# Optimization experiments

Hardware: AMD Instinct MI355X
Metric: run time of the kernel (lower is better)

Reference implementation:

```python
import jax, jax.numpy as jnp
import numpy as np

# Fixed generation configuration (original samples num_nodes per graph from
# dataset stats; here batched with fixed node count so shapes are static).
B, N = 64, 384                 # num_graphs, nodes per graph
NOISE, CED, HID, FEAT, NCLS = 128, 64, 512, 256, 10
DENSITY = 0.05                 # fallback density used by the original code
TEMP = 1.0                     # temperature
IU, JU = np.triu_indices(N, k=1)   # all i<j pairs, matches nested loop order
P = IU.shape[0]                # pairs per graph = N*(N-1)/2
K = int(round(DENSITY * P))    # topk edges per graph


def setup_inputs() -> dict:
    key = jax.random.key(0)
    ks = jax.random.split(key, 8)
    f32 = jnp.float32
    return {
        "z": jax.random.normal(ks[0], (B, N, NOISE), f32),
        "class_labels": jax.random.randint(ks[1], (B,), 0, NCLS),
        "embed_table": jax.random.normal(ks[2], (NCLS, CED), f32),
        "W1": jax.random.normal(ks[3], (NOISE + CED, HID), f32) / np.float32(np.sqrt(NOISE + CED)),
        "b1": jnp.zeros((HID,), f32),
        "W2": jax.random.normal(ks[4], (HID, FEAT), f32) / np.float32(np.sqrt(HID)),
        "b2": jnp.zeros((FEAT,), f32),
        "We": jax.random.normal(ks[5], (FEAT, HID), f32) / np.float32(np.sqrt(FEAT)),
        "be": jnp.zeros((HID,), f32),
        "threshold": jnp.float32(1.0),
    }


def reference(z, class_labels, embed_table, W1, b1, W2, b2, We, be, threshold):
    # class embedding, broadcast to every node of the graph
    ce = embed_table[class_labels]                               # [B, CED]
    ce = jnp.broadcast_to(ce[:, None, :], (B, N, CED))
    inp = jnp.concatenate([z, ce], axis=-1)                      # [B, N, NOISE+CED]
    # node generator: Linear -> ReLU -> Linear
    x = jax.nn.relu(inp @ W1 + b1) @ W2 + b2                     # [B, N, FEAT]
    # edge predictor encoder: Linear -> ReLU
    h = jax.nn.relu(x @ We + be)                                 # [B, N, HID]
    # pairwise L2 distances via gram trick (replaces O(n^2) torch.norm loop)
    sq = jnp.sum(h * h, axis=-1)                                 # [B, N]
    gram = jnp.einsum('bnd,bmd->bnm', h, h)                      # [B, N, N]
    d2 = jnp.maximum(sq[:, :, None] + sq[:, None, :] - 2.0 * gram, 0.0)
    dist = jnp.sqrt(jnp.maximum(d2[:, IU, JU], 1e-12))           # [B, P] upper-tri pairs
    probs = jax.nn.sigmoid((threshold - dist) / max(TEMP, 1e-6)) # [B, P]
    # per-graph top-k edge selection
    top_probs, top_idx = jax.lax.top_k(probs, K)                 # [B, K]
    iu = jnp.asarray(IU, jnp.int32)
    ju = jnp.asarray(JU, jnp.int32)
    offs = (jnp.arange(B, dtype=jnp.int32) * N)[:, None]         # node offset per graph
    u = iu[top_idx] + offs                                       # [B, K]
    v = ju[top_idx] + offs
    # per graph: [[u, v], [v, u]] (symmetrized), graphs concatenated
    row0 = jnp.concatenate([u, v], axis=1).reshape(-1)           # [B*2K]
    row1 = jnp.concatenate([v, u], axis=1).reshape(-1)
    edge_index = jnp.stack([row0, row1], axis=0)                 # [2, B*2K]
    batch = jnp.repeat(jnp.arange(B, dtype=jnp.int32), N)        # [B*N]
    return x.reshape(B * N, FEAT), edge_index, batch, top_probs
```

## Files before the change

kernel.cpp:

```cpp
#include <hip/hip_runtime.h>
#include <hip/hip_bf16.h>

#define NB    64
#define NN    384
#define PPAIR 73536
#define PRECT 147456
#define KSEL  3677
#define NSLICE 8
#define SLICEK (PRECT / NSLICE)

#define OFF_X 0
#define OFF_E 6291456
#define B2K   470656
#define OFF_B 7232768
#define OFF_P 7257344
#define TOT   7492672

#define WS_H8    0ull
#define WS_GH    0ull
#define WS_SB    4194304ull
#define WS_SQ    12582912ull
#define WS_W1P   12681216ull
#define WS_W2P   12877824ull
#define WS_WEP   13139968ull
#define WS_KEY   13402112ull
#define WS_SEL   38567936ull
#define WS_TB    39509248ull

typedef __attribute__((ext_vector_type(8))) short bf16x8;
typedef __attribute__((ext_vector_type(4))) float f32x4;

__device__ __forceinline__ short f2bf(float f) {
    __hip_bfloat16 h = __float2bfloat16(f);
    return *reinterpret_cast<short*>(&h);
}
__device__ __forceinline__ unsigned enc8(float h) {
    if (!(h > 0.0078125f)) return 0u;
    unsigned u = __float_as_uint(h) + 0x00080000u;
    int E = (int)(u >> 23) - 127;
    if (E > 8)  return 0x7Eu;
    if (E < -6) return 0u;
    return (unsigned)(((E + 7) << 3) | ((u >> 20) & 7u));
}
__device__ __forceinline__ float dec8(unsigned b) {
    if (b == 0u) return 0.f;
    return __uint_as_float((((b >> 3) + 120u) << 23) | ((b & 7u) << 20));
}

__device__ __forceinline__ void bar_lds() {
    asm volatile("s_waitcnt lgkmcnt(0)\n\ts_barrier" ::: "memory");
}

__device__ __forceinline__ int4 pack8bf(const float4& A, const float4& B) {
    int4 v;
    v.x = (unsigned short)f2bf(A.x) | ((unsigned)(unsigned short)f2bf(A.y) << 16);
    v.y = (unsigned short)f2bf(A.z) | ((unsigned)(unsigned short)f2bf(A.w) << 16);
    v.z = (unsigned short)f2bf(B.x) | ((unsigned)(unsigned short)f2bf(B.y) << 16);
    v.w = (unsigned short)f2bf(B.z) | ((unsigned)(unsigned short)f2bf(B.w) << 16);
    return v;
}

__device__ __forceinline__ void packOne(
    const float* __restrict__ W, int K, int N, short* __restrict__ dst, int idx)
{
    if (idx >= K * N) return;
    int j = idx & 7;
    int l = (idx >> 3) & 63;
    int rest = idx >> 9;
    int Kt = K >> 5;
    int kt = rest % Kt, mt = rest / Kt;
    int k = kt * 32 + (l >> 4) * 8 + j;
    int n = mt * 16 + (l & 15);
    dst[idx] = f2bf(W[(size_t)k * N + n]);
}

__global__ __launch_bounds__(256) void pack_all_kernel(
    const float* __restrict__ W1, const float* __restrict__ W2,
    const float* __restrict__ We, short* __restrict__ W1p,
    short* __restrict__ W2p, short* __restrict__ Wep, float* __restrict__ sqW)
{
    int blk = blockIdx.x, tid = threadIdx.x;
    if (blk < 384)        packOne(W1, 192, 512, W1p, blk * 256 + tid);
    else if (blk < 896)   packOne(W2, 512, 256, W2p, (blk - 384) * 256 + tid);
    else if (blk < 1408)  packOne(We, 256, 512, Wep, (blk - 896) * 256 + tid);
    else {
        int i = (blk - 1408) * 256 + tid;
        if (i < NB * NN) sqW[i] = 0.f;
    }
}

__global__ __launch_bounds__(256, 3) void fused_mlp_kernel(
    const float* __restrict__ z, const int* __restrict__ cls,
    const float* __restrict__ et,
    const short* __restrict__ W1p, const float* __restrict__ b1,
    const short* __restrict__ W2p, const float* __restrict__ b2,
    const short* __restrict__ Wep, const float* __restrict__ be,
    float* __restrict__ xOut, unsigned char* __restrict__ h8Out,
    float* __restrict__ sqOut)
{
    extern __shared__ short lds[];
    short* A_lds  = lds;
    short* t1_lds = lds + 6400;
    short* x_lds  = lds;

    const int tid = threadIdx.x;
    const int r0 = blockIdx.x * 32;
    const int lane = tid & 63;
    const int l15 = lane & 15, kj = lane >> 4;
    const int w = tid >> 6;
    const int cl = cls[r0 / NN];

    {
        const int row = tid >> 3, c8 = tid & 7;
        float4 LA0, LB0, LA1, LB1;
        auto ld = [&](int kc, float4& A, float4& B) {
            int col = kc * 64 + c8 * 8;
            if (col < 128) {
                const float* src = z + (size_t)(r0 + row) * 128 + col;
                A = *(const float4*)src; B = *(const float4*)(src + 4);
            } else {
                const float* src = et + cl * 64 + (col - 128);
                A = *(const float4*)src; B = *(const float4*)(src + 4);
            }
        };
        auto st = [&](int kc, const float4& A, const float4& B) {
            *(int4*)(A_lds + row * 200 + kc * 64 + c8 * 8) = pack8bf(A, B);
        };
        ld(0, LA0, LB0);
        ld(1, LA1, LB1);
        st(0, LA0, LB0);
        ld(2, LA0, LB0);
        st(1, LA1, LB1);
        st(2, LA0, LB0);
    }
    bar_lds();

    f32x4 acc2[4][2];
#pragma unroll
    for (int t = 0; t < 4; ++t)
#pragma unroll
        for (int s = 0; s < 2; ++s) acc2[t][s] = (f32x4){0.f, 0.f, 0.f, 0.f};

    for (int ft = 0; ft < 4; ++ft) {
        f32x4 acc1[2][2];
#pragma unroll
        for (int t = 0; t < 2; ++t)
#pragma unroll
            for (int s = 0; s < 2; ++s) acc1[t][s] = (f32x4){0.f, 0.f, 0.f, 0.f};

#pragma unroll
        for (int kt = 0; kt < 6; ++kt) {
            bf16x8 aF[2], bF[2];
#pragma unroll
            for (int t = 0; t < 2; ++t) {
                int mt = ft * 8 + w * 2 + t;
                aF[t] = *(const bf16x8*)(W1p + ((size_t)(mt * 6 + kt) << 9) + (lane << 3));
            }
#pragma unroll
            for (int s = 0; s < 2; ++s)
                bF[s] = *(const bf16x8*)(A_lds + (s * 16 + l15) * 200 + kt * 32 + (kj << 3));
#pragma unroll
            for (int t = 0; t < 2; ++t)
#pragma unroll
                for (int s = 0; s < 2; ++s)
                    acc1[t][s] = __builtin_amdgcn_mfma_f32_16x16x32_bf16(aF[t], bF[s], acc1[t][s], 0, 0, 0);
        }
#pragma unroll
        for (int t = 0; t < 2; ++t) {
            int fl = (w * 2 + t) * 16 + (kj << 2);
            float4 bv = *(const float4*)(b1 + ft * 128 + fl);
#pragma unroll
            for (int s = 0; s < 2; ++s) {
                int node = s * 16 + l15;
                f32x4 a = acc1[t][s];
                float v0 = fmaxf(a.x + bv.x, 0.f), v1 = fmaxf(a.y + bv.y, 0.f);
                float v2 = fmaxf(a.z + bv.z, 0.f), v3 = fmaxf(a.w + bv.w, 0.f);
                int2 pk;
                pk.x = (unsigned short)f2bf(v0) | ((unsigned)(unsigned short)f2bf(v1) << 16);
                pk.y = (unsigned short)f2bf(v2) | ((unsigned)(unsigned short)f2bf(v3) << 16);
                *(int2*)(t1_lds + node * 136 + fl) = pk;
            }
        }
        bar_lds();
#pragma unroll
        for (int kt2 = 0; kt2 < 4; ++kt2) {
            int kt = ft * 4 + kt2;
            bf16x8 bF[2];
#pragma unroll
            for (int s = 0; s < 2; ++s)
                bF[s] = *(const bf16x8*)(t1_lds + (s * 16 + l15) * 136 + kt2 * 32 + (kj << 3));
#pragma unroll
            for (int t = 0; t < 4; ++t) {
                int mt = w * 4 + t;
                bf16x8 aF = *(const bf16x8*)(W2p + ((size_t)(mt * 16 + kt) << 9) + (lane << 3));
#pragma unroll
                for (int s = 0; s < 2; ++s)
                    acc2[t][s] = __builtin_amdgcn_mfma_f32_16x16x32_bf16(aF, bF[s], acc2[t][s], 0, 0, 0);
            }
        }
        bar_lds();
    }

#pragma unroll
    for (int t = 0; t < 4; ++t) {
        int feat = w * 64 + t * 16 + (kj << 2);
        float4 bv = *(const float4*)(b2 + feat);
#pragma unroll
        for (int s = 0; s < 2; ++s) {
            int node = s * 16 + l15;
            f32x4 a = acc2[t][s];
            float v0 = a.x + bv.x, v1 = a.y + bv.y;
            float v2 = a.z + bv.z, v3 = a.w + bv.w;
            float4 o; o.x = v0; o.y = v1; o.z = v2; o.w = v3;
            *(float4*)(xOut + (size_t)(r0 + node) * 256 + feat) = o;
            int2 pk;
            pk.x = (unsigned short)f2bf(v0) | ((unsigned)(unsigned short)f2bf(v1) << 16);
            pk.y = (unsigned short)f2bf(v2) | ((unsigned)(unsigned short)f2bf(v3) << 16);
            *(int2*)(x_lds + node * 264 + feat) = pk;
        }
    }
    bar_lds();

    for (int ft3 = 0; ft3 < 4; ++ft3) {
        f32x4 acc[2][2];
#pragma unroll
        for (int t = 0; t < 2; ++t)
#pragma unroll
            for (int s = 0; s < 2; ++s) acc[t][s] = (f32x4){0.f, 0.f, 0.f, 0.f};

#pragma unroll
        for (int kt = 0; kt < 8; ++kt) {
            bf16x8 aF[2], bF[2];
#pragma unroll
            for (int t = 0; t < 2; ++t) {
                int mt = ft3 * 8 + w * 2 + t;
                aF[t] = *(const bf16x8*)(Wep + ((size_t)(mt * 8 + kt) << 9) + (lane << 3));
            }
#pragma unroll
            for (int s = 0; s < 2; ++s)
                bF[s] = *(const bf16x8*)(x_lds + (s * 16 + l15) * 264 + kt * 32 + (kj << 3));
#pragma unroll
            for (int t = 0; t < 2; ++t)
#pragma unroll
                for (int s = 0; s < 2; ++s)
                    acc[t][s] = __builtin_amdgcn_mfma_f32_16x16x32_bf16(aF[t], bF[s], acc[t][s], 0, 0, 0);
        }
        float sqp[2] = {0.f, 0.f};
#pragma unroll
        for (int t = 0; t < 2; ++t) {
            int feat = ft3 * 128 + (w * 2 + t) * 16 + (kj << 2);
            float4 bv = *(const float4*)(be + feat);
#pragma unroll
            for (int s = 0; s < 2; ++s) {
                int node = s * 16 + l15;
                f32x4 a = acc[t][s];
                float v0 = fmaxf(a.x + bv.x, 0.f), v1 = fmaxf(a.y + bv.y, 0.f);
                float v2 = fmaxf(a.z + bv.z, 0.f), v3 = fmaxf(a.w + bv.w, 0.f);
                unsigned e0 = enc8(v0), e1 = enc8(v1), e2 = enc8(v2), e3 = enc8(v3);
                *(unsigned*)(h8Out + (size_t)(r0 + node) * 512 + feat) =
                    e0 | (e1 << 8) | (e2 << 16) | (e3 << 24);
                float h0 = dec8(e0), h1 = dec8(e1), h2 = dec8(e2), h3 = dec8(e3);
                sqp[s] += h0 * h0 + h1 * h1 + h2 * h2 + h3 * h3;
            }
        }
#pragma unroll
        for (int s = 0; s < 2; ++s) {
            float v = sqp[s];
            v += __shfl_xor(v, 16);
            v += __shfl_xor(v, 32);
            if (kj == 0)
                atomicAdd(sqOut + r0 + s * 16 + l15, v);
        }
    }
}

__global__ __launch_bounds__(256) void gram_mfma_kernel(
    const unsigned char* __restrict__ hW8, const float* __restrict__ sqW,
    unsigned short* __restrict__ keyW)
{
    extern __shared__ unsigned char smem8[];
    unsigned char* As = smem8;
    unsigned char* Bs = smem8 + 16896;

    const int tid = threadIdx.x;
    const int b  = blockIdx.x;
    int tp = blockIdx.y;
    int ti = 0; { int rem = tp; while (rem >= 6 - ti) { rem -= 6 - ti; ++ti; } tp = rem; }
    const int tj = ti + tp;
    const bool diag = (ti == tj);
    const unsigned char* Bp = diag ? As : Bs;

    const int w = tid >> 6;
    const int lane = tid & 63;
    const int l15 = lane & 15, kj = lane >> 4;
    const int mb = w * 16;

    f32x4 acc[4];
#pragma unroll
    for (int t = 0; t < 4; ++t) acc[t] = (f32x4){0.f, 0.f, 0.f, 0.f};

    const size_t baseA = ((size_t)b * NN + ti * 64) * 512;
    const size_t baseB = ((size_t)b * NN + tj * 64) * 512;

    int4 pa[4], pb[4];
    auto issue = [&](int kc) {
#pragma unroll
        for (int q = 0; q < 4; ++q) {
            int i = tid + (q << 8);
            int row = i >> 4, g = i & 15;
            pa[q] = *(const int4*)(hW8 + baseA + row * 512 + kc * 256 + g * 16);
            if (!diag)
                pb[q] = *(const int4*)(hW8 + baseB + row * 512 + kc * 256 + g * 16);
        }
    };
    auto store = [&]() {
#pragma unroll
        for (int q = 0; q < 4; ++q) {
            int i = tid + (q << 8);
            int row = i >> 4, g = i & 15;
            *(int4*)(As + row * 264 + g * 16) = pa[q];
            if (!diag) *(int4*)(Bs + row * 264 + g * 16) = pb[q];
        }
    };

    issue(0);
    for (int kc = 0; kc < 2; ++kc) {
        store();
        if (kc == 0) issue(1);
        bar_lds();
#pragma unroll
        for (int kt = 0; kt < 8; ++kt) {
            long long aF = *(const long long*)(As + (mb + l15) * 264 + kt * 32 + kj * 8);
#pragma unroll
            for (int nt = 0; nt < 4; ++nt) {
                long long bF = *(const long long*)(Bp + (nt * 16 + l15) * 264 + kt * 32 + kj * 8);
                acc[nt] = __builtin_amdgcn_mfma_f32_16x16x32_fp8_fp8(aF, bF, acc[nt], 0, 0, 0);
            }
        }
        bar_lds();
    }

    unsigned short* tile = (unsigned short*)smem8;
    float4 sqi = *(const float4*)(sqW + b * NN + ti * 64 + mb + kj * 4);
    float si[4] = { sqi.x, sqi.y, sqi.z, sqi.w };
#pragma unroll
    for (int nt = 0; nt < 4; ++nt) {
        int colL = nt * 16 + l15;
        float sj = sqW[b * NN + tj * 64 + colL];
        float av[4] = { acc[nt].x, acc[nt].y, acc[nt].z, acc[nt].w };
#pragma unroll
        for (int r = 0; r < 4; ++r) {
            int rowL = mb + kj * 4 + r;
            float d2 = fmaxf(si[r] + sj - 2.f * av[r], 0.f);
            unsigned short key = (unsigned short)(__float_as_uint(d2) >> 16);
            bool valid = !diag || (rowL < colL);
            tile[rowL * 72 + colL] = valid ? key : (unsigned short)0xFFFF;
        }
    }
    bar_lds();
#pragma unroll
    for (int it = 0; it < 2; ++it) {
        int idx = tid + (it << 8);
        int row = idx >> 3, c8 = idx & 7;
        int4 v = *(const int4*)(tile + row * 72 + c8 * 8);
        *(int4*)(keyW + (size_t)b * PRECT + (size_t)(ti * 64 + row) * NN
                 + tj * 64 + c8 * 8) = v;
    }
}

__global__ __launch_bounds__(1024) void selA_kernel(
    const unsigned short* __restrict__ keyW, unsigned short* __restrict__ ghist)
{
    const int b = blockIdx.x, s = blockIdx.y, tid = threadIdx.x;
    const unsigned short* keys = keyW + (size_t)b * PRECT + (size_t)s * SLICEK;
    __shared__ unsigned hist[4096];
    for (int i = tid; i < 4096; i += 1024) hist[i] = 0;
    __syncthreads();
    for (int p = tid; p < SLICEK; p += 1024) {
        unsigned k = keys[p];
        if (k < 0x8000u) atomicAdd(&hist[k >> 4], 1u);
    }
    __syncthreads();
    unsigned short* dst = ghist + ((size_t)(b * NSLICE + s) << 12);
    for (int i = tid; i < 4096; i += 1024) dst[i] = (unsigned short)hist[i];
}

__global__ __launch_bounds__(1024) void selB_kernel(
    const unsigned short* __restrict__ ghist, unsigned* __restrict__ sliceBase,
    unsigned* __restrict__ Tbuf)
{
    const int b = blockIdx.x, tid = threadIdx.x;
    __shared__ unsigned base[4096];
    __shared__ unsigned scanBuf[1024];
    __shared__ int sTc;
    if (tid == 0) sTc = 4095;

    unsigned c[4]; unsigned tsum = 0;
#pragma unroll
    for (int q = 0; q < 4; ++q) {
        int bin = tid * 4 + q;
        unsigned v = 0;
        for (int s = 0; s < NSLICE; ++s)
            v += ghist[((size_t)(b * NSLICE + s) << 12) + bin];
        c[q] = v; tsum += v;
    }
    scanBuf[tid] = tsum;
    __syncthreads();
    for (int o = 1; o < 1024; o <<= 1) {
        unsigned v = (tid >= o) ? scanBuf[tid - o] : 0u;
        __syncthreads();
        scanBuf[tid] += v;
        __syncthreads();
    }
    unsigned exc = scanBuf[tid] - tsum;
    {
        unsigned run = exc;
#pragma unroll
        for (int q = 0; q < 4; ++q) { base[tid * 4 + q] = run; run += c[q]; }
    }
    __syncthreads();
#pragma unroll
    for (int q = 0; q < 4; ++q) {
        int i = tid * 4 + q;
        if (base[i] < KSEL && base[i] + c[q] >= KSEL) atomicMin(&sTc, i);
    }
    __syncthreads();
    if (tid == 0) Tbuf[b] = (unsigned)sTc;

#pragma unroll
    for (int q = 0; q < 4; ++q) {
        int bin = tid * 4 + q;
        unsigned runb = base[bin];
        for (int s = 0; s < NSLICE; ++s) {
            size_t off = ((size_t)(b * NSLICE + s) << 12) + bin;
            sliceBase[off] = runb;
            runb += ghist[off];
        }
    }
}

__global__ __launch_bounds__(1024) void selC_kernel(
    const unsigned short* __restrict__ keyW, const unsigned* __restrict__ sliceBase,
    const unsigned* __restrict__ Tbuf, unsigned* __restrict__ selP)
{
    const int b = blockIdx.x, s = blockIdx.y, tid = threadIdx.x;
    const unsigned short* keys = keyW + (size_t)b * PRECT + (size_t)s * SLICEK;
    __shared__ unsigned cnt[4096];
    const unsigned* src = sliceBase + ((size_t)(b * NSLICE + s) << 12);
    for (int i = tid; i < 4096; i += 1024) cnt[i] = src[i];
    __syncthreads();
    int T = (int)Tbuf[b];
    for (int p = tid; p < SLICEK; p += 1024) {
        unsigned k = keys[p];
        if (k < 0x8000u) {
            int bin = k >> 4;
            if (bin <= T) {
                unsigned pos = atomicAdd(&cnt[bin], 1u);
                if (pos < KSEL)
                    selP[(size_t)b * KSEL + pos] = (unsigned)(s * SLICEK + p);
            }
        }
    }
}

__global__ __launch_bounds__(256) void emit_kernel(
    const unsigned short* __restrict__ keyW, const unsigned* __restrict__ selP,
    const float* __restrict__ thrp, float* __restrict__ outF)
{
    long long idx = OFF_E + (long long)blockIdx.x * 256 + threadIdx.x;
    if (idx >= TOT) return;

    if (idx < OFF_B) {
        long long q = idx - OFF_E;
        int row = (int)(q / B2K);
        int rem = (int)(q - (long long)row * B2K);
        int b = rem / (2 * KSEL);
        int t = rem - b * (2 * KSEL);
        int slot = (t < KSEL) ? t : (t - KSEL);
        unsigned p = selP[(size_t)b * KSEL + slot];
        if (p >= PRECT) p = 1;
        int i = p / NN;
        int j = p - i * NN;
        bool first = (t < KSEL);
        int node = (row == 0) ? (first ? i : j) : (first ? j : i);
        outF[idx] = (float)(b * NN + node);
        return;
    }
    if (idx < OFF_P) {
        int m = (int)(idx - OFF_B);
        outF[idx] = (float)(m / NN);
        return;
    }
    {
        int m = (int)(idx - OFF_P);
        int b = m / KSEL;
        int k = m - b * KSEL;
        unsigned p = selP[(size_t)b * KSEL + k];
        if (p >= PRECT) p = 1;
        unsigned short key = keyW[(size_t)b * PRECT + p];
        float d2 = __uint_as_float(((unsigned)key) << 16);
        float dist = sqrtf(fmaxf(d2, 1e-12f));
        outF[idx] = 1.0f / (1.0f + expf(dist - thrp[0]));
    }
}

extern "C" void kernel_launch(void* const* d_in, const int* in_sizes, int n_in,
                              void* d_out, int out_size, void* d_ws, size_t ws_size,
                              hipStream_t stream) {
    (void)in_sizes; (void)n_in; (void)out_size; (void)ws_size;
    const float* z   = (const float*)d_in[0];
    const int*   cls = (const int*)d_in[1];
    const float* et  = (const float*)d_in[2];
    const float* W1  = (const float*)d_in[3];
    const float* b1  = (const float*)d_in[4];
    const float* W2  = (const float*)d_in[5];
    const float* b2  = (const float*)d_in[6];
    const float* We  = (const float*)d_in[7];
    const float* be  = (const float*)d_in[8];
    const float* thr = (const float*)d_in[9];
    float* outF = (float*)d_out;

    char* w = (char*)d_ws;
    unsigned char*  hW8   = (unsigned char*)(w + WS_H8);
    float*          sqW   = (float*)(w + WS_SQ);
    short*          W1p   = (short*)(w + WS_W1P);
    short*          W2p   = (short*)(w + WS_W2P);
    short*          Wep   = (short*)(w + WS_WEP);
    unsigned short* keyW  = (unsigned short*)(w + WS_KEY);
    unsigned*       selP  = (unsigned*)(w + WS_SEL);
    unsigned short* ghist = (unsigned short*)(w + WS_GH);
    unsigned*       sbase = (unsigned*)(w + WS_SB);
    unsigned*       Tbuf  = (unsigned*)(w + WS_TB);

    pack_all_kernel<<<1504, 256, 0, stream>>>(W1, W2, We, W1p, W2p, Wep, sqW);

    fused_mlp_kernel<<<768, 256, 21504, stream>>>(
        z, cls, et, W1p, b1, W2p, b2, Wep, be, outF + OFF_X, hW8, sqW);

    gram_mfma_kernel<<<dim3(64, 21), 256, 33792, stream>>>(hW8, sqW, keyW);
    selA_kernel<<<dim3(64, NSLICE), 1024, 0, stream>>>(keyW, ghist);
    selB_kernel<<<64, 1024, 0, stream>>>(ghist, sbase, Tbuf);
    selC_kernel<<<dim3(64, NSLICE), 1024, 0, stream>>>(keyW, sbase, Tbuf, selP);
    int emitN = TOT - OFF_E;
    emit_kernel<<<(emitN + 255) / 256, 256, 0, stream>>>(keyW, selP, thr, outF);
}
```

Before: 197.6 us.

## Merge selection kernels into one cooperative launch and halve MLP row tile

Replaces the four selection and emit launches (histogram, scan, scatter, emit) with a single cooperative kernel that uses grid-wide syncs between phases. Launch gaps and per-kernel ramp-up are the costs it targets. The fused MLP kernel now handles 16 rows per block instead of 32, with static LDS and a higher occupancy bound, giving twice as many blocks. In exchange, the grid syncs cost time, 256 persistent blocks give less parallelism in each phase, and the smaller row tile loads the weight fragments twice as often.

```diff
diff --git a/kernel.cpp b/kernel.cpp
--- a/kernel.cpp
+++ b/kernel.cpp
@@ -1,5 +1,8 @@
 #include <hip/hip_runtime.h>
 #include <hip/hip_bf16.h>
+#include <hip/hip_cooperative_groups.h>
+
+namespace cg = cooperative_groups;
 
 #define NB    64
 #define NN    384
@@ -51,13 +54,11 @@
     asm volatile("s_waitcnt lgkmcnt(0)\n\ts_barrier" ::: "memory");
 }
 
-__device__ __forceinline__ int4 pack8bf(const float4& A, const float4& B) {
-    int4 v;
-    v.x = (unsigned short)f2bf(A.x) | ((unsigned)(unsigned short)f2bf(A.y) << 16);
-    v.y = (unsigned short)f2bf(A.z) | ((unsigned)(unsigned short)f2bf(A.w) << 16);
-    v.z = (unsigned short)f2bf(B.x) | ((unsigned)(unsigned short)f2bf(B.y) << 16);
-    v.w = (unsigned short)f2bf(B.z) | ((unsigned)(unsigned short)f2bf(B.w) << 16);
-    return v;
+__device__ __forceinline__ int2 pack4bf(float a, float b, float c, float d) {
+    int2 pk;
+    pk.x = (unsigned short)f2bf(a) | ((unsigned)(unsigned short)f2bf(b) << 16);
+    pk.y = (unsigned short)f2bf(c) | ((unsigned)(unsigned short)f2bf(d) << 16);
+    return pk;
 }
 
 __device__ __forceinline__ void packOne(
@@ -89,7 +90,7 @@
     }
 }
 
-__global__ __launch_bounds__(256, 3) void fused_mlp_kernel(
+__global__ __launch_bounds__(256, 6) void fused_mlp_kernel(
     const float* __restrict__ z, const int* __restrict__ cls,
     const float* __restrict__ et,
     const short* __restrict__ W1p, const float* __restrict__ b1,
@@ -98,104 +99,78 @@
     float* __restrict__ xOut, unsigned char* __restrict__ h8Out,
     float* __restrict__ sqOut)
 {
-    extern __shared__ short lds[];
+    __shared__ short lds[5376];
     short* A_lds  = lds;
-    short* t1_lds = lds + 6400;
+    short* t1_lds = lds + 3200;
     short* x_lds  = lds;
 
     const int tid = threadIdx.x;
-    const int r0 = blockIdx.x * 32;
+    const int r0 = blockIdx.x * 16;
     const int lane = tid & 63;
     const int l15 = lane & 15, kj = lane >> 4;
     const int w = tid >> 6;
     const int cl = cls[r0 / NN];
 
     {
-        const int row = tid >> 3, c8 = tid & 7;
-        float4 LA0, LB0, LA1, LB1;
-        auto ld = [&](int kc, float4& A, float4& B) {
-            int col = kc * 64 + c8 * 8;
-            if (col < 128) {
-                const float* src = z + (size_t)(r0 + row) * 128 + col;
-                A = *(const float4*)src; B = *(const float4*)(src + 4);
-            } else {
-                const float* src = et + cl * 64 + (col - 128);
-                A = *(const float4*)src; B = *(const float4*)(src + 4);
-            }
-        };
-        auto st = [&](int kc, const float4& A, const float4& B) {
-            *(int4*)(A_lds + row * 200 + kc * 64 + c8 * 8) = pack8bf(A, B);
-        };
-        ld(0, LA0, LB0);
-        ld(1, LA1, LB1);
-        st(0, LA0, LB0);
-        ld(2, LA0, LB0);
-        st(1, LA1, LB1);
-        st(2, LA0, LB0);
+        float4 v[3];
+#pragma unroll
+        for (int q = 0; q < 3; ++q) {
+            int u = tid + q * 256;
+            int row = u / 48, c4 = u - row * 48;
+            int col = c4 * 4;
+            const float* src = (col < 128)
+                ? (z + (size_t)(r0 + row) * 128 + col)
+                : (et + cl * 64 + (col - 128));
+            v[q] = *(const float4*)src;
+        }
+#pragma unroll
+        for (int q = 0; q < 3; ++q) {
+            int u = tid + q * 256;
+            int row = u / 48, c4 = u - row * 48;
+            *(int2*)(A_lds + row * 200 + c4 * 4) =
+                pack4bf(v[q].x, v[q].y, v[q].z, v[q].w);
+        }
     }
     bar_lds();
 
-    f32x4 acc2[4][2];
-#pragma unroll
-    for (int t = 0; t < 4; ++t)
-#pragma unroll
-        for (int s = 0; s < 2; ++s) acc2[t][s] = (f32x4){0.f, 0.f, 0.f, 0.f};
+    f32x4 acc2[4];
+#pragma unroll
+    for (int t = 0; t < 4; ++t) acc2[t] = (f32x4){0.f, 0.f, 0.f, 0.f};
 
     for (int ft = 0; ft < 4; ++ft) {
-        f32x4 acc1[2][2];
-#pragma unroll
-        for (int t = 0; t < 2; ++t)
-#pragma unroll
-            for (int s = 0; s < 2; ++s) acc1[t][s] = (f32x4){0.f, 0.f, 0.f, 0.f};
+        f32x4 acc1[2];
+#pragma unroll
+        for (int t = 0; t < 2; ++t) acc1[t] = (f32x4){0.f, 0.f, 0.f, 0.f};
 
 #pragma unroll
         for (int kt = 0; kt < 6; ++kt) {
-            bf16x8 aF[2], bF[2];
+            bf16x8 bF = *(const bf16x8*)(A_lds + l15 * 200 + kt * 32 + (kj << 3));
 #pragma unroll
             for (int t = 0; t < 2; ++t) {
                 int mt = ft * 8 + w * 2 + t;
-                aF[t] = *(const bf16x8*)(W1p + ((size_t)(mt * 6 + kt) << 9) + (lane << 3));
+                bf16x8 aF = *(const bf16x8*)(W1p + ((size_t)(mt * 6 + kt) << 9) + (lane << 3));
+                acc1[t] = __builtin_amdgcn_mfma_f32_16x16x32_bf16(aF, bF, acc1[t], 0, 0, 0);
             }
-#pragma unroll
-            for (int s = 0; s < 2; ++s)
-                bF[s] = *(const bf16x8*)(A_lds + (s * 16 + l15) * 200 + kt * 32 + (kj << 3));
-#pragma unroll
-            for (int t = 0; t < 2; ++t)
-#pragma unroll
-                for (int s = 0; s < 2; ++s)
-                    acc1[t][s] = __builtin_amdgcn_mfma_f32_16x16x32_bf16(aF[t], bF[s], acc1[t][s], 0, 0, 0);
         }
 #pragma unroll
         for (int t = 0; t < 2; ++t) {
             int fl = (w * 2 + t) * 16 + (kj << 2);
             float4 bv = *(const float4*)(b1 + ft * 128 + fl);
-#pragma unroll
-            for (int s = 0; s < 2; ++s) {
-                int node = s * 16 + l15;
-                f32x4 a = acc1[t][s];
-                float v0 = fmaxf(a.x + bv.x, 0.f), v1 = fmaxf(a.y + bv.y, 0.f);
-                float v2 = fmaxf(a.z + bv.z, 0.f), v3 = fmaxf(a.w + bv.w, 0.f);
-                int2 pk;
-                pk.x = (unsigned short)f2bf(v0) | ((unsigned)(unsigned short)f2bf(v1) << 16);
-                pk.y = (unsigned short)f2bf(v2) | ((unsigned)(unsigned short)f2bf(v3) << 16);
-                *(int2*)(t1_lds + node * 136 + fl) = pk;
-            }
+            f32x4 a = acc1[t];
+            float v0 = fmaxf(a.x + bv.x, 0.f), v1 = fmaxf(a.y + bv.y, 0.f);
+            float v2 = fmaxf(a.z + bv.z, 0.f), v3 = fmaxf(a.w + bv.w, 0.f);
+            *(int2*)(t1_lds + l15 * 136 + fl) = pack4bf(v0, v1, v2, v3);
         }
         bar_lds();
 #pragma unroll
         for (int kt2 = 0; kt2 < 4; ++kt2) {
             int kt = ft * 4 + kt2;
-            bf16x8 bF[2];
-#pragma unroll
-            for (int s = 0; s < 2; ++s)
-                bF[s] = *(const bf16x8*)(t1_lds + (s * 16 + l15) * 136 + kt2 * 32 + (kj << 3));
+            bf16x8 bF = *(const bf16x8*)(t1_lds + l15 * 136 + kt2 * 32 + (kj << 3));
 #pragma unroll
             for (int t = 0; t < 4; ++t) {
                 int mt = w * 4 + t;
                 bf16x8 aF = *(const bf16x8*)(W2p + ((size_t)(mt * 16 + kt) << 9) + (lane << 3));
-#pragma unroll
-                for (int s = 0; s < 2; ++s)
-                    acc2[t][s] = __builtin_amdgcn_mfma_f32_16x16x32_bf16(aF, bF[s], acc2[t][s], 0, 0, 0);
+                acc2[t] = __builtin_amdgcn_mfma_f32_16x16x32_bf16(aF, bF, acc2[t], 0, 0, 0);
             }
         }
         bar_lds();
@@ -205,73 +180,49 @@
     for (int t = 0; t < 4; ++t) {
         int feat = w * 64 + t * 16 + (kj << 2);
         float4 bv = *(const float4*)(b2 + feat);
-#pragma unroll
-        for (int s = 0; s < 2; ++s) {
-            int node = s * 16 + l15;
-            f32x4 a = acc2[t][s];
-            float v0 = a.x + bv.x, v1 = a.y + bv.y;
-            float v2 = a.z + bv.z, v3 = a.w + bv.w;
-            float4 o; o.x = v0; o.y = v1; o.z = v2; o.w = v3;
-            *(float4*)(xOut + (size_t)(r0 + node) * 256 + feat) = o;
-            int2 pk;
-            pk.x = (unsigned short)f2bf(v0) | ((unsigned)(unsigned short)f2bf(v1) << 16);
-            pk.y = (unsigned short)f2bf(v2) | ((unsigned)(unsigned short)f2bf(v3) << 16);
-            *(int2*)(x_lds + node * 264 + feat) = pk;
-        }
+        f32x4 a = acc2[t];
+        float v0 = a.x + bv.x, v1 = a.y + bv.y;
+        float v2 = a.z + bv.z, v3 = a.w + bv.w;
+        float4 o; o.x = v0; o.y = v1; o.z = v2; o.w = v3;
+        *(float4*)(xOut + (size_t)(r0 + l15) * 256 + feat) = o;
+        *(int2*)(x_lds + l15 * 264 + feat) = pack4bf(v0, v1, v2, v3);
     }
     bar_lds();
 
+    float sqp = 0.f;
     for (int ft3 = 0; ft3 < 4; ++ft3) {
-        f32x4 acc[2][2];
-#pragma unroll
-        for (int t = 0; t < 2; ++t)
-#pragma unroll
-            for (int s = 0; s < 2; ++s) acc[t][s] = (f32x4){0.f, 0.f, 0.f, 0.f};
+        f32x4 acc[2];
+#pragma unroll
+        for (int t = 0; t < 2; ++t) acc[t] = (f32x4){0.f, 0.f, 0.f, 0.f};
 
 #pragma unroll
         for (int kt = 0; kt < 8; ++kt) {
-            bf16x8 aF[2], bF[2];
+            bf16x8 bF = *(const bf16x8*)(x_lds + l15 * 264 + kt * 32 + (kj << 3));
 #pragma unroll
             for (int t = 0; t < 2; ++t) {
                 int mt = ft3 * 8 + w * 2 + t;
-                aF[t] = *(const bf16x8*)(Wep + ((size_t)(mt * 8 + kt) << 9) + (lane << 3));
+                bf16x8 aF = *(const bf16x8*)(Wep + ((size_t)(mt * 8 + kt) << 9) + (lane << 3));
+                acc[t] = __builtin_amdgcn_mfma_f32_16x16x32_bf16(aF, bF, acc[t], 0, 0, 0);
             }
-#pragma unroll
-            for (int s = 0; s < 2; ++s)
-                bF[s] = *(const bf16x8*)(x_lds + (s * 16 + l15) * 264 + kt * 32 + (kj << 3));
-#pragma unroll
-            for (int t = 0; t < 2; ++t)
-#pragma unroll
-                for (int s = 0; s < 2; ++s)
-                    acc[t][s] = __builtin_amdgcn_mfma_f32_16x16x32_bf16(aF[t], bF[s], acc[t][s], 0, 0, 0);
-        }
-        float sqp[2] = {0.f, 0.f};
+        }
 #pragma unroll
         for (int t = 0; t < 2; ++t) {
             int feat = ft3 * 128 + (w * 2 + t) * 16 + (kj << 2);
             float4 bv = *(const float4*)(be + feat);
-#pragma unroll
-            for (int s = 0; s < 2; ++s) {
-                int node = s * 16 + l15;
-                f32x4 a = acc[t][s];
-                float v0 = fmaxf(a.x + bv.x, 0.f), v1 = fmaxf(a.y + bv.y, 0.f);
-                float v2 = fmaxf(a.z + bv.z, 0.f), v3 = fmaxf(a.w + bv.w, 0.f);
-                unsigned e0 = enc8(v0), e1 = enc8(v1), e2 = enc8(v2), e3 = enc8(v3);
-                *(unsigned*)(h8Out + (size_t)(r0 + node) * 512 + feat) =
-                    e0 | (e1 << 8) | (e2 << 16) | (e3 << 24);
-                float h0 = dec8(e0), h1 = dec8(e1), h2 = dec8(e2), h3 = dec8(e3);
-                sqp[s] += h0 * h0 + h1 * h1 + h2 * h2 + h3 * h3;
-            }
-        }
-#pragma unroll
-        for (int s = 0; s < 2; ++s) {
-            float v = sqp[s];
-            v += __shfl_xor(v, 16);
-            v += __shfl_xor(v, 32);
-            if (kj == 0)
-                atomicAdd(sqOut + r0 + s * 16 + l15, v);
-        }
-    }
+            f32x4 a = acc[t];
+            float v0 = fmaxf(a.x + bv.x, 0.f), v1 = fmaxf(a.y + bv.y, 0.f);
+            float v2 = fmaxf(a.z + bv.z, 0.f), v3 = fmaxf(a.w + bv.w, 0.f);
+            unsigned e0 = enc8(v0), e1 = enc8(v1), e2 = enc8(v2), e3 = enc8(v3);
+            *(unsigned*)(h8Out + (size_t)(r0 + l15) * 512 + feat) =
+                e0 | (e1 << 8) | (e2 << 16) | (e3 << 24);
+            float h0 = dec8(e0), h1 = dec8(e1), h2 = dec8(e2), h3 = dec8(e3);
+            sqp += h0 * h0 + h1 * h1 + h2 * h2 + h3 * h3;
+        }
+    }
+    sqp += __shfl_xor(sqp, 16);
+    sqp += __shfl_xor(sqp, 32);
+    if (kj == 0)
+        atomicAdd(sqOut + r0 + l15, sqp);
 }
 
 __global__ __launch_bounds__(256) void gram_mfma_kernel(
@@ -365,6 +316,137 @@
         int4 v = *(const int4*)(tile + row * 72 + c8 * 8);
         *(int4*)(keyW + (size_t)b * PRECT + (size_t)(ti * 64 + row) * NN
                  + tj * 64 + c8 * 8) = v;
+    }
+}
+
+__global__ __launch_bounds__(1024) void select_all_kernel(
+    const unsigned short* __restrict__ keyW, unsigned short* __restrict__ ghist,
+    unsigned* __restrict__ sliceBase, unsigned* __restrict__ Tbuf,
+    const float* __restrict__ thrp, unsigned* __restrict__ selP,
+    float* __restrict__ outF)
+{
+    cg::grid_group gg = cg::this_grid();
+    __shared__ unsigned hist[4096];
+    __shared__ unsigned scanBuf[1024];
+    __shared__ int sTc;
+    const int tid = threadIdx.x;
+    const int blk = blockIdx.x;
+
+    for (int unit = blk; unit < NB * NSLICE; unit += 256) {
+        const int b = unit >> 3, s = unit & 7;
+        const unsigned short* keys = keyW + (size_t)b * PRECT + (size_t)s * SLICEK;
+        for (int i = tid; i < 4096; i += 1024) hist[i] = 0;
+        __syncthreads();
+        for (int p = tid; p < SLICEK; p += 1024) {
+            unsigned k = keys[p];
+            if (k < 0x8000u) atomicAdd(&hist[k >> 4], 1u);
+        }
+        __syncthreads();
+        unsigned short* dst = ghist + ((size_t)unit << 12);
+        for (int i = tid; i < 4096; i += 1024) dst[i] = (unsigned short)hist[i];
+        __syncthreads();
+    }
+    gg.sync();
+
+    if (blk < NB) {
+        const int b = blk;
+        if (tid == 0) sTc = 4095;
+        unsigned c[4]; unsigned tsum = 0;
+#pragma unroll
+        for (int q = 0; q < 4; ++q) {
+            int bin = tid * 4 + q;
+            unsigned v = 0;
+            for (int s = 0; s < NSLICE; ++s)
+                v += ghist[((size_t)(b * NSLICE + s) << 12) + bin];
+            c[q] = v; tsum += v;
+        }
+        scanBuf[tid] = tsum;
+        __syncthreads();
+        for (int o = 1; o < 1024; o <<= 1) {
+            unsigned v = (tid >= o) ? scanBuf[tid - o] : 0u;
+            __syncthreads();
+            scanBuf[tid] += v;
+            __syncthreads();
+        }
+        unsigned exc = scanBuf[tid] - tsum;
+        {
+            unsigned run = exc;
+#pragma unroll
+            for (int q = 0; q < 4; ++q) { hist[tid * 4 + q] = run; run += c[q]; }
+        }
+        __syncthreads();
+#pragma unroll
+        for (int q = 0; q < 4; ++q) {
+            int i = tid * 4 + q;
+            if (hist[i] < KSEL && hist[i] + c[q] >= KSEL) atomicMin(&sTc, i);
+        }
+        __syncthreads();
+        if (tid == 0) Tbuf[b] = (unsigned)sTc;
+#pragma unroll
+        for (int q = 0; q < 4; ++q) {
+            int bin = tid * 4 + q;
+            unsigned runb = hist[bin];
+            for (int s = 0; s < NSLICE; ++s) {
+                size_t off = ((size_t)(b * NSLICE + s) << 12) + bin;
+                sliceBase[off] = runb;
+                runb += ghist[off];
+            }
+        }
+    }
+    gg.sync();
+
+    for (int unit = blk; unit < NB * NSLICE; unit += 256) {
+        const int b = unit >> 3, s = unit & 7;
+        const unsigned short* keys = keyW + (size_t)b * PRECT + (size_t)s * SLICEK;
+        const unsigned* src = sliceBase + ((size_t)unit << 12);
+        for (int i = tid; i < 4096; i += 1024) hist[i] = src[i];
+        __syncthreads();
+        int T = (int)Tbuf[b];
+        for (int p = tid; p < SLICEK; p += 1024) {
+            unsigned k = keys[p];
+            if (k < 0x8000u) {
+                int bin = k >> 4;
+                if (bin <= T) {
+                    unsigned pos = atomicAdd(&hist[bin], 1u);
+                    if (pos < KSEL)
+                        selP[(size_t)b * KSEL + pos] = (unsigned)(s * SLICEK + p);
+                }
+            }
+        }
+        __syncthreads();
+    }
+    gg.sync();
+
+    for (long long idx = OFF_E + (long long)blk * 1024 + tid; idx < TOT;
+         idx += 256LL * 1024) {
+        if (idx < OFF_B) {
+            long long q = idx - OFF_E;
+            int row = (int)(q / B2K);
+            int rem = (int)(q - (long long)row * B2K);
+            int b = rem / (2 * KSEL);
+            int t = rem - b * (2 * KSEL);
+            int slot = (t < KSEL) ? t : (t - KSEL);
+            unsigned p = selP[(size_t)b * KSEL + slot];
+            if (p >= PRECT) p = 1;
+            int i = p / NN;
+            int j = p - i * NN;
+            bool first = (t < KSEL);
+            int node = (row == 0) ? (first ? i : j) : (first ? j : i);
+            outF[idx] = (float)(b * NN + node);
+        } else if (idx < OFF_P) {
+            int m = (int)(idx - OFF_B);
+            outF[idx] = (float)(m / NN);
+        } else {
+            int m = (int)(idx - OFF_P);
+            int b = m / KSEL;
+            int k = m - b * KSEL;
+            unsigned p = selP[(size_t)b * KSEL + k];
+            if (p >= PRECT) p = 1;
+            unsigned short key = keyW[(size_t)b * PRECT + p];
+            float d2 = __uint_as_float(((unsigned)key) << 16);
+            float dist = sqrtf(fmaxf(d2, 1e-12f));
+            outF[idx] = 1.0f / (1.0f + expf(dist - thrp[0]));
+        }
     }
 }
 
@@ -534,13 +616,22 @@
 
     pack_all_kernel<<<1504, 256, 0, stream>>>(W1, W2, We, W1p, W2p, Wep, sqW);
 
-    fused_mlp_kernel<<<768, 256, 21504, stream>>>(
+    fused_mlp_kernel<<<1536, 256, 0, stream>>>(
         z, cls, et, W1p, b1, W2p, b2, Wep, be, outF + OFF_X, hW8, sqW);
 
     gram_mfma_kernel<<<dim3(64, 21), 256, 33792, stream>>>(hW8, sqW, keyW);
-    selA_kernel<<<dim3(64, NSLICE), 1024, 0, stream>>>(keyW, ghist);
-    selB_kernel<<<64, 1024, 0, stream>>>(ghist, sbase, Tbuf);
-    selC_kernel<<<dim3(64, NSLICE), 1024, 0, stream>>>(keyW, sbase, Tbuf, selP);
-    int emitN = TOT - OFF_E;
-    emit_kernel<<<(emitN + 255) / 256, 256, 0, stream>>>(keyW, selP, thr, outF);
-}
+
+    {
+        void* args[] = { (void*)&keyW, (void*)&ghist, (void*)&sbase,
+                         (void*)&Tbuf, (void*)&thr, (void*)&selP, (void*)&outF };
+        hipError_t e = hipLaunchCooperativeKernel(
+            (const void*)select_all_kernel, dim3(256), dim3(1024), args, 0, stream);
+        if (e != hipSuccess) {
+            selA_kernel<<<dim3(64, NSLICE), 1024, 0, stream>>>(keyW, ghist);
+            selB_kernel<<<64, 1024, 0, stream>>>(ghist, sbase, Tbuf);
+            selC_kernel<<<dim3(64, NSLICE), 1024, 0, stream>>>(keyW, sbase, Tbuf, selP);
+            int emitN = TOT - OFF_E;
+            emit_kernel<<<(emitN + 255) / 256, 256, 0, stream>>>(keyW, selP, thr, outF);
+        }
+    }
+}
```

Result: slower. 330.7 us (+67.4%).

## Widen fused MLP to 512 threads and drop the chunked layer-1/layer-2 loop

Applied to the files above, without the earlier changes.

Runs the fused MLP block with 8 waves instead of 4. Each wave now computes its full share of the 512 hidden features of layer 1 in a single pass and stores them to a larger LDS buffer, and layer 2 then reduces over K=512 in one loop. This replaces the four-chunk interleave and removes its per-chunk barriers. The change also uses static shared memory (about 45KB) and sets launch bounds of 512 threads with a minimum of 6 blocks, which limits register usage per thread and may cause spills or lower occupancy.

```diff
diff --git a/kernel.cpp b/kernel.cpp
--- a/kernel.cpp
+++ b/kernel.cpp
@@ -51,13 +51,11 @@
     asm volatile("s_waitcnt lgkmcnt(0)\n\ts_barrier" ::: "memory");
 }
 
-__device__ __forceinline__ int4 pack8bf(const float4& A, const float4& B) {
-    int4 v;
-    v.x = (unsigned short)f2bf(A.x) | ((unsigned)(unsigned short)f2bf(A.y) << 16);
-    v.y = (unsigned short)f2bf(A.z) | ((unsigned)(unsigned short)f2bf(A.w) << 16);
-    v.z = (unsigned short)f2bf(B.x) | ((unsigned)(unsigned short)f2bf(B.y) << 16);
-    v.w = (unsigned short)f2bf(B.z) | ((unsigned)(unsigned short)f2bf(B.w) << 16);
-    return v;
+__device__ __forceinline__ int2 pack4bf(float a, float b, float c, float d) {
+    int2 pk;
+    pk.x = (unsigned short)f2bf(a) | ((unsigned)(unsigned short)f2bf(b) << 16);
+    pk.y = (unsigned short)f2bf(c) | ((unsigned)(unsigned short)f2bf(d) << 16);
+    return pk;
 }
 
 __device__ __forceinline__ void packOne(
@@ -89,7 +87,7 @@
     }
 }
 
-__global__ __launch_bounds__(256, 3) void fused_mlp_kernel(
+__global__ __launch_bounds__(512, 6) void fused_mlp_kernel(
     const float* __restrict__ z, const int* __restrict__ cls,
     const float* __restrict__ et,
     const short* __restrict__ W1p, const float* __restrict__ b1,
@@ -98,7 +96,7 @@
     float* __restrict__ xOut, unsigned char* __restrict__ h8Out,
     float* __restrict__ sqOut)
 {
-    extern __shared__ short lds[];
+    __shared__ short lds[23040];
     short* A_lds  = lds;
     short* t1_lds = lds + 6400;
     short* x_lds  = lds;
@@ -111,99 +109,91 @@
     const int cl = cls[r0 / NN];
 
     {
-        const int row = tid >> 3, c8 = tid & 7;
-        float4 LA0, LB0, LA1, LB1;
-        auto ld = [&](int kc, float4& A, float4& B) {
-            int col = kc * 64 + c8 * 8;
-            if (col < 128) {
-                const float* src = z + (size_t)(r0 + row) * 128 + col;
-                A = *(const float4*)src; B = *(const float4*)(src + 4);
-            } else {
-                const float* src = et + cl * 64 + (col - 128);
-                A = *(const float4*)src; B = *(const float4*)(src + 4);
-            }
-        };
-        auto st = [&](int kc, const float4& A, const float4& B) {
-            *(int4*)(A_lds + row * 200 + kc * 64 + c8 * 8) = pack8bf(A, B);
-        };
-        ld(0, LA0, LB0);
-        ld(1, LA1, LB1);
-        st(0, LA0, LB0);
-        ld(2, LA0, LB0);
-        st(1, LA1, LB1);
-        st(2, LA0, LB0);
+        float4 v[3];
+#pragma unroll
+        for (int q = 0; q < 3; ++q) {
+            int u = tid + q * 512;
+            int row = u / 48, c4 = u - row * 48;
+            int col = c4 * 4;
+            const float* src = (col < 128)
+                ? (z + (size_t)(r0 + row) * 128 + col)
+                : (et + cl * 64 + (col - 128));
+            v[q] = *(const float4*)src;
+        }
+#pragma unroll
+        for (int q = 0; q < 3; ++q) {
+            int u = tid + q * 512;
+            int row = u / 48, c4 = u - row * 48;
+            *(int2*)(A_lds + row * 200 + c4 * 4) =
+                pack4bf(v[q].x, v[q].y, v[q].z, v[q].w);
+        }
     }
     bar_lds();
 
-    f32x4 acc2[4][2];
-#pragma unroll
-    for (int t = 0; t < 4; ++t)
-#pragma unroll
-        for (int s = 0; s < 2; ++s) acc2[t][s] = (f32x4){0.f, 0.f, 0.f, 0.f};
-
-    for (int ft = 0; ft < 4; ++ft) {
-        f32x4 acc1[2][2];
-#pragma unroll
-        for (int t = 0; t < 2; ++t)
-#pragma unroll
-            for (int s = 0; s < 2; ++s) acc1[t][s] = (f32x4){0.f, 0.f, 0.f, 0.f};
+    {
+        f32x4 acc1[4][2];
+#pragma unroll
+        for (int m = 0; m < 4; ++m)
+#pragma unroll
+            for (int s = 0; s < 2; ++s) acc1[m][s] = (f32x4){0.f, 0.f, 0.f, 0.f};
 
 #pragma unroll
         for (int kt = 0; kt < 6; ++kt) {
-            bf16x8 aF[2], bF[2];
-#pragma unroll
-            for (int t = 0; t < 2; ++t) {
-                int mt = ft * 8 + w * 2 + t;
-                aF[t] = *(const bf16x8*)(W1p + ((size_t)(mt * 6 + kt) << 9) + (lane << 3));
-            }
+            bf16x8 bF[2];
 #pragma unroll
             for (int s = 0; s < 2; ++s)
                 bF[s] = *(const bf16x8*)(A_lds + (s * 16 + l15) * 200 + kt * 32 + (kj << 3));
 #pragma unroll
-            for (int t = 0; t < 2; ++t)
+            for (int m = 0; m < 4; ++m) {
+                int mt = w * 4 + m;
+                bf16x8 aF = *(const bf16x8*)(W1p + ((size_t)(mt * 6 + kt) << 9) + (lane << 3));
 #pragma unroll
                 for (int s = 0; s < 2; ++s)
-                    acc1[t][s] = __builtin_amdgcn_mfma_f32_16x16x32_bf16(aF[t], bF[s], acc1[t][s], 0, 0, 0);
-        }
-#pragma unroll
-        for (int t = 0; t < 2; ++t) {
-            int fl = (w * 2 + t) * 16 + (kj << 2);
-            float4 bv = *(const float4*)(b1 + ft * 128 + fl);
+                    acc1[m][s] = __builtin_amdgcn_mfma_f32_16x16x32_bf16(aF, bF[s], acc1[m][s], 0, 0, 0);
+            }
+        }
+#pragma unroll
+        for (int m = 0; m < 4; ++m) {
+            int fl = (w * 4 + m) * 16 + (kj << 2);
+            float4 bv = *(const float4*)(b1 + fl);
 #pragma unroll
             for (int s = 0; s < 2; ++s) {
                 int node = s * 16 + l15;
-                f32x4 a = acc1[t][s];
+                f32x4 a = acc1[m][s];
                 float v0 = fmaxf(a.x + bv.x, 0.f), v1 = fmaxf(a.y + bv.y, 0.f);
                 float v2 = fmaxf(a.z + bv.z, 0.f), v3 = fmaxf(a.w + bv.w, 0.f);
-                int2 pk;
-                pk.x = (unsigned short)f2bf(v0) | ((unsigned)(unsigned short)f2bf(v1) << 16);
-                pk.y = (unsigned short)f2bf(v2) | ((unsigned)(unsigned short)f2bf(v3) << 16);
-                *(int2*)(t1_lds + node * 136 + fl) = pk;
+                *(int2*)(t1_lds + node * 520 + fl) = pack4bf(v0, v1, v2, v3);
             }
         }
-        bar_lds();
-#pragma unroll
-        for (int kt2 = 0; kt2 < 4; ++kt2) {
-            int kt = ft * 4 + kt2;
-            bf16x8 bF[2];
+    }
+    bar_lds();
+
+    f32x4 acc2[2][2];
+#pragma unroll
+    for (int t = 0; t < 2; ++t)
+#pragma unroll
+        for (int s = 0; s < 2; ++s) acc2[t][s] = (f32x4){0.f, 0.f, 0.f, 0.f};
+
+#pragma unroll
+    for (int kt = 0; kt < 16; ++kt) {
+        bf16x8 bF[2];
+#pragma unroll
+        for (int s = 0; s < 2; ++s)
+            bF[s] = *(const bf16x8*)(t1_lds + (s * 16 + l15) * 520 + kt * 32 + (kj << 3));
+#pragma unroll
+        for (int t = 0; t < 2; ++t) {
+            int mt = w * 2 + t;
+            bf16x8 aF = *(const bf16x8*)(W2p + ((size_t)(mt * 16 + kt) << 9) + (lane << 3));
 #pragma unroll
             for (int s = 0; s < 2; ++s)
-                bF[s] = *(const bf16x8*)(t1_lds + (s * 16 + l15) * 136 + kt2 * 32 + (kj << 3));
-#pragma unroll
-            for (int t = 0; t < 4; ++t) {
-                int mt = w * 4 + t;
-                bf16x8 aF = *(const bf16x8*)(W2p + ((size_t)(mt * 16 + kt) << 9) + (lane << 3));
-#pragma unroll
-                for (int s = 0; s < 2; ++s)
-                    acc2[t][s] = __builtin_amdgcn_mfma_f32_16x16x32_bf16(aF, bF[s], acc2[t][s], 0, 0, 0);
-            }
-        }
-        bar_lds();
-    }
-
-#pragma unroll
-    for (int t = 0; t < 4; ++t) {
-        int feat = w * 64 + t * 16 + (kj << 2);
+                acc2[t][s] = __builtin_amdgcn_mfma_f32_16x16x32_bf16(aF, bF[s], acc2[t][s], 0, 0, 0);
+        }
+    }
+    bar_lds();
+
+#pragma unroll
+    for (int t = 0; t < 2; ++t) {
+        int feat = (w * 2 + t) * 16 + (kj << 2);
         float4 bv = *(const float4*)(b2 + feat);
 #pragma unroll
         for (int s = 0; s < 2; ++s) {
@@ -213,47 +203,42 @@
             float v2 = a.z + bv.z, v3 = a.w + bv.w;
             float4 o; o.x = v0; o.y = v1; o.z = v2; o.w = v3;
             *(float4*)(xOut + (size_t)(r0 + node) * 256 + feat) = o;
-            int2 pk;
-            pk.x = (unsigned short)f2bf(v0) | ((unsigned)(unsigned short)f2bf(v1) << 16);
-            pk.y = (unsigned short)f2bf(v2) | ((unsigned)(unsigned short)f2bf(v3) << 16);
-            *(int2*)(x_lds + node * 264 + feat) = pk;
+            *(int2*)(x_lds + node * 264 + feat) = pack4bf(v0, v1, v2, v3);
         }
     }
     bar_lds();
 
-    for (int ft3 = 0; ft3 < 4; ++ft3) {
-        f32x4 acc[2][2];
-#pragma unroll
-        for (int t = 0; t < 2; ++t)
-#pragma unroll
-            for (int s = 0; s < 2; ++s) acc[t][s] = (f32x4){0.f, 0.f, 0.f, 0.f};
+    {
+        f32x4 acc3[4][2];
+#pragma unroll
+        for (int m = 0; m < 4; ++m)
+#pragma unroll
+            for (int s = 0; s < 2; ++s) acc3[m][s] = (f32x4){0.f, 0.f, 0.f, 0.f};
 
 #pragma unroll
         for (int kt = 0; kt < 8; ++kt) {
-            bf16x8 aF[2], bF[2];
-#pragma unroll
-            for (int t = 0; t < 2; ++t) {
-                int mt = ft3 * 8 + w * 2 + t;
-                aF[t] = *(const bf16x8*)(Wep + ((size_t)(mt * 8 + kt) << 9) + (lane << 3));
-            }
+            bf16x8 bF[2];
 #pragma unroll
             for (int s = 0; s < 2; ++s)
                 bF[s] = *(const bf16x8*)(x_lds + (s * 16 + l15) * 264 + kt * 32 + (kj << 3));
 #pragma unroll
-            for (int t = 0; t < 2; ++t)
+            for (int m = 0; m < 4; ++m) {
+                int mt = w * 4 + m;
+                bf16x8 aF = *(const bf16x8*)(Wep + ((size_t)(mt * 8 + kt) << 9) + (lane << 3));
 #pragma unroll
                 for (int s = 0; s < 2; ++s)
-                    acc[t][s] = __builtin_amdgcn_mfma_f32_16x16x32_bf16(aF[t], bF[s], acc[t][s], 0, 0, 0);
+                    acc3[m][s] = __builtin_amdgcn_mfma_f32_16x16x32_bf16(aF, bF[s], acc3[m][s], 0, 0, 0);
+            }
         }
         float sqp[2] = {0.f, 0.f};
 #pragma unroll
-        for (int t = 0; t < 2; ++t) {
-            int feat = ft3 * 128 + (w * 2 + t) * 16 + (kj << 2);
+        for (int m = 0; m < 4; ++m) {
+            int feat = (w * 4 + m) * 16 + (kj << 2);
             float4 bv = *(const float4*)(be + feat);
 #pragma unroll
             for (int s = 0; s < 2; ++s) {
                 int node = s * 16 + l15;
-                f32x4 a = acc[t][s];
+                f32x4 a = acc3[m][s];
                 float v0 = fmaxf(a.x + bv.x, 0.f), v1 = fmaxf(a.y + bv.y, 0.f);
                 float v2 = fmaxf(a.z + bv.z, 0.f), v3 = fmaxf(a.w + bv.w, 0.f);
                 unsigned e0 = enc8(v0), e1 = enc8(v1), e2 = enc8(v2), e3 = enc8(v3);
@@ -534,7 +519,7 @@
 
     pack_all_kernel<<<1504, 256, 0, stream>>>(W1, W2, We, W1p, W2p, Wep, sqW);
 
-    fused_mlp_kernel<<<768, 256, 21504, stream>>>(
+    fused_mlp_kernel<<<768, 512, 0, stream>>>(
         z, cls, et, W1p, b1, W2p, b2, Wep, be, outF + OFF_X, hW8, sqW);
 
     gram_mfma_kernel<<<dim3(64, 21), 256, 33792, stream>>>(hW8, sqW, keyW);
```

Measured after the change: 200.5 us. Within noise of the previous version (+1.5%).
